# Performance work log

Measured on AMD Instinct MI355X. Metric: run time of the kernel, lower is better.

Reference implementation:

```python
import jax, jax.numpy as jnp
from jax import lax
import numpy as np

DIM = 128
HEADS = 2
WS = 4            # window_size = int(44 / 11)
HIDDEN = 4 * DIM  # ffn_expansion_factor = 4


def setup_inputs() -> dict:
    key = jax.random.key(0)
    ks = jax.random.split(key, 16)
    b, c, h, w = 4, DIM, 88, 88
    s = 0.02
    return {
        "x": jax.random.normal(ks[0], (b, c, h, w), jnp.float32),
        "mask": jax.random.uniform(ks[1], (b, 1, 44, 44), jnp.float32),
        "edge_f": jax.random.normal(ks[2], (b, c, 44, 44), jnp.float32),
        "ln1_w": jnp.ones((c,), jnp.float32),
        "ln1_b": jnp.zeros((c,), jnp.float32),
        "Wq": jax.random.normal(ks[3], (c, c), jnp.float32) * s,
        "Wk": jax.random.normal(ks[4], (c, c), jnp.float32) * s,
        "Wv": jax.random.normal(ks[5], (c, c), jnp.float32) * s,
        "ln2_w": jnp.ones((c,), jnp.float32),
        "ln2_b": jnp.zeros((c,), jnp.float32),
        "w_in": jax.random.normal(ks[6], (2 * HIDDEN, c), jnp.float32) * s,      # 1x1 conv dim -> 2*hidden
        "w_dw": jax.random.normal(ks[7], (2 * HIDDEN, 1, 3, 3), jnp.float32) * s,  # depthwise 3x3
        "w_out": jax.random.normal(ks[8], (c, HIDDEN), jnp.float32) * s,          # 1x1 conv hidden -> dim
    }


def _layernorm_c(t, g, beta):
    # WithBias LayerNorm over the channel axis (to_3d normalizes last dim == c)
    mu = t.mean(axis=1, keepdims=True)
    var = t.var(axis=1, keepdims=True)
    return (t - mu) / jnp.sqrt(var + 1e-5) * g[None, :, None, None] + beta[None, :, None, None]


def _windows(t, ws):
    # (b,c,h,w) -> (b*h*w/ws^2, ws^2, c), matching torch view/permute/contiguous
    b, c, h, w = t.shape
    t = t.reshape(b, c, h // ws, ws, w // ws, ws)
    t = t.transpose(0, 2, 4, 3, 5, 1)  # b, h/ws, w/ws, ws, ws, c
    return t.reshape(-1, ws * ws, c)


def reference(x, mask, edge_f, ln1_w, ln1_b, Wq, Wk, Wv, ln2_w, ln2_b, w_in, w_dw, w_out):
    b, c, h, w = x.shape
    ws, heads = WS, HEADS
    dh = c // heads
    scale = dh ** (-0.5)

    # ---- Attention branch (norm1 -> windowed edge/mask-conditioned attention) ----
    xn = _layernorm_c(x, ln1_w, ln1_b)
    edge = jax.image.resize(edge_f, (b, c, h, w), method="bilinear")
    m = jax.image.resize(mask, (b, mask.shape[1], h, w), method="bilinear")

    q = _windows(edge, ws) @ Wq.T            # (Bw, ws^2, c); dropout inactive (eval)
    x0 = _windows(xn * m, ws)                # mask-modulated keys/values
    k = x0 @ Wk.T
    v = x0 @ Wv.T

    Bw = q.shape[0]
    q = q.reshape(Bw, ws * ws, heads, dh)
    k = k.reshape(Bw, ws * ws, heads, dh)
    v = v.reshape(Bw, ws * ws, heads, dh)

    # dots: per-token head_dim x head_dim matrix, summed over heads (as in the source einsum)
    dots = jnp.einsum("bnhj,bnhk->bnjk", q, k) * scale   # (Bw, ws^2, dh, dh)
    attn = jax.nn.softmax(dots, axis=-1)
    out = jnp.einsum("bnjk,bnhk->bnhj", attn, v)          # (Bw, ws^2, heads, dh)

    out = out.reshape(Bw, ws * ws, c)
    out = out.reshape(b, h // ws, w // ws, ws * ws * c)
    out = out.transpose(0, 3, 1, 2).reshape(b, c, h, w)   # scrambled view, faithful to source

    x = x + out

    # ---- FeedForward branch (norm2 -> gated dwconv FFN) ----
    xn2 = _layernorm_c(x, ln2_w, ln2_b)
    t = jnp.einsum("oc,bchw->bohw", w_in, xn2)            # 1x1 conv, no bias
    t = lax.conv_general_dilated(
        t, w_dw, (1, 1), "SAME",
        feature_group_count=w_dw.shape[0],
        dimension_numbers=("NCHW", "OIHW", "NCHW"))
    t1, t2 = jnp.split(t, 2, axis=1)
    t = jax.nn.gelu(t1, approximate=False) * t2
    out2 = jnp.einsum("oc,bchw->bohw", w_out, t)
    return x + out2
```

## Files before the change

### kernel.cpp

```cpp
#include <hip/hip_runtime.h>
#include <hip/hip_bf16.h>
#include <math.h>

#define BATCH 4
#define C 128
#define H 88
#define W 88
#define HW 7744
#define NPIX 30976
#define HALF 44
#define HID 512

#if defined(__has_builtin)
#  if __has_builtin(__builtin_amdgcn_exp2f)
#    define EXP_FAST(x) __builtin_amdgcn_exp2f(x)
#    define QSCALE 0.18033688011112042f
#  endif
#endif
#ifndef EXP_FAST
#  define EXP_FAST(x) __expf(x)
#  define QSCALE 0.125f
#endif

typedef __attribute__((ext_vector_type(8))) short bfrag;
typedef __attribute__((ext_vector_type(4))) float f32x4;

__device__ __forceinline__ short f2bf(float f) {
    union { __hip_bfloat16 b; unsigned short u; } cv;
    cv.b = __float2bfloat16(f);
    return (short)cv.u;
}
__device__ __forceinline__ float bf2f(short s) {
    union { unsigned int u; float f; } cv;
    cv.u = ((unsigned int)(unsigned short)s) << 16;
    return cv.f;
}
__device__ __forceinline__ bfrag cvt8(const float* p) {
    const float4 f0 = *(const float4*)p;
    const float4 f1 = *(const float4*)(p + 4);
    bfrag t;
    t[0] = f2bf(f0.x); t[1] = f2bf(f0.y); t[2] = f2bf(f0.z); t[3] = f2bf(f0.w);
    t[4] = f2bf(f1.x); t[5] = f2bf(f1.y); t[6] = f2bf(f1.z); t[7] = f2bf(f1.w);
    return t;
}

__device__ __forceinline__ void up_taps(int i, int& j0, int& j1, float& w0, float& w1) {
    float f = 0.5f * i - 0.25f;
    int i0 = (int)floorf(f);
    float fr = f - (float)i0;
    j0 = max(i0, 0);
    j1 = min(i0 + 1, HALF - 1);
    w0 = 1.f - fr;
    w1 = fr;
}

__global__ __launch_bounds__(256) void k_pre(
    const float* __restrict__ x, const float* __restrict__ mask,
    const float* __restrict__ edge, const float* __restrict__ ln1w,
    const float* __restrict__ ln1b,
    __hip_bfloat16* __restrict__ xnm, __hip_bfloat16* __restrict__ eo)
{
    __shared__ float redS[8][32], redQ[8][32];
    const int tid = threadIdx.x, s = tid >> 5, px = tid & 31;
    const int blk = blockIdx.x, b = blk / 242, hw0 = (blk % 242) * 32;
    const int hw = hw0 + px, hi = hw / W, wi = hw % W;
    const int cs = s * 16;

    int y0, y1, x0, x1c; float wy0, wy1, wx0, wx1;
    up_taps(hi, y0, y1, wy0, wy1);
    up_taps(wi, x0, x1c, wx0, wx1);

    const float* mb = mask + (size_t)b * HALF * HALF;
    const float mval = wy0 * (wx0 * mb[y0 * HALF + x0] + wx1 * mb[y0 * HALF + x1c])
                     + wy1 * (wx0 * mb[y1 * HALF + x0] + wx1 * mb[y1 * HALF + x1c]);

    const float* xb = x + (size_t)b * C * HW;
    const float* ebs = edge + (size_t)b * C * HALF * HALF;
    float xr[16], er[16];
    float sum = 0.f, sq = 0.f;
    #pragma unroll
    for (int i = 0; i < 16; ++i) {
        const int c = cs + i;
        const float t = xb[c * HW + hw];
        xr[i] = t; sum += t; sq += t * t;
        const float* ec = ebs + c * HALF * HALF;
        er[i] = wy0 * (wx0 * ec[y0 * HALF + x0] + wx1 * ec[y0 * HALF + x1c])
              + wy1 * (wx0 * ec[y1 * HALF + x0] + wx1 * ec[y1 * HALF + x1c]);
    }
    redS[s][px] = sum; redQ[s][px] = sq;
    __syncthreads();
    float tsum = 0.f, tsq = 0.f;
    #pragma unroll
    for (int i = 0; i < 8; ++i) { tsum += redS[i][px]; tsq += redQ[i][px]; }
    const float mu = tsum * (1.f / C);
    const float rstd = rsqrtf(tsq * (1.f / C) - mu * mu + 1e-5f);

    const size_t gp = (size_t)b * HW + hw;
    bfrag r0, r1;
    #pragma unroll
    for (int i = 0; i < 8; ++i) {
        r0[i] = f2bf(((xr[i] - mu) * rstd * ln1w[cs + i] + ln1b[cs + i]) * mval);
        r1[i] = f2bf(((xr[8 + i] - mu) * rstd * ln1w[cs + 8 + i] + ln1b[cs + 8 + i]) * mval);
    }
    *(bfrag*)((short*)xnm + gp * C + cs) = r0;
    *(bfrag*)((short*)xnm + gp * C + cs + 8) = r1;
    #pragma unroll
    for (int i = 0; i < 8; ++i) { r0[i] = f2bf(er[i]); r1[i] = f2bf(er[8 + i]); }
    *(bfrag*)((short*)eo + gp * C + cs) = r0;
    *(bfrag*)((short*)eo + gp * C + cs + 8) = r1;
}


__global__ __launch_bounds__(512) void k_gemmQKV(
    const __hip_bfloat16* __restrict__ eb, const __hip_bfloat16* __restrict__ xnm,
    const float* __restrict__ Wq, const float* __restrict__ Wk, const float* __restrict__ Wv,
    __hip_bfloat16* __restrict__ qb, __hip_bfloat16* __restrict__ kb,
    __hip_bfloat16* __restrict__ vb)
{
    __shared__ short Bs[64 * 136];
    const int mat = blockIdx.y >> 1;
    const int c0 = (blockIdx.y & 1) * 64;
    const __hip_bfloat16* A; const float* Wf; __hip_bfloat16* Out;
    if (mat == 0)      { A = eb;  Wf = Wq; Out = qb; }
    else if (mat == 1) { A = xnm; Wf = Wk; Out = kb; }
    else               { A = xnm; Wf = Wv; Out = vb; }

    const int tid = threadIdx.x;
    {
        const int sr = tid & 63, sq = tid >> 6;
        const float* wr = Wf + (size_t)(c0 + sr) * 128 + sq * 16;
        short* dstS = &Bs[sr * 136 + sq * 16];
        *(bfrag*)dstS = cvt8(wr);
        *(bfrag*)(dstS + 8) = cvt8(wr + 8);
    }
    __syncthreads();

    const int lane = tid & 63, wv = tid >> 6;
    const int wm = wv & 3, wn = wv >> 2;
    const int px0 = blockIdx.x * 128 + wm * 32;
    const int lcb = wn * 32;
    const int lr = lane & 15, lg = lane >> 4;
    const short* As = (const short*)A;

    f32x4 acc[2][2];
    #pragma unroll
    for (int i = 0; i < 2; ++i)
        #pragma unroll
        for (int j = 0; j < 2; ++j)
            #pragma unroll
            for (int r = 0; r < 4; ++r) acc[i][j][r] = 0.f;

    bfrag a_[4][2], b_[2][2];
    #pragma unroll
    for (int ks = 0; ks < 4; ++ks)
        #pragma unroll
        for (int mi = 0; mi < 2; ++mi)
            a_[ks][mi] = *(const bfrag*)(As + (size_t)(px0 + mi * 16 + lr) * 128 + ks * 32 + lg * 8);
    #pragma unroll
    for (int nj = 0; nj < 2; ++nj)
        b_[0][nj] = *(const bfrag*)&Bs[(lcb + nj * 16 + lr) * 136 + lg * 8];

    #pragma unroll
    for (int ks = 0; ks < 4; ++ks) {
        if (ks < 3) {
            #pragma unroll
            for (int nj = 0; nj < 2; ++nj)
                b_[(ks + 1) & 1][nj] = *(const bfrag*)&Bs[(lcb + nj * 16 + lr) * 136 + (ks + 1) * 32 + lg * 8];
        }
        #pragma unroll
        for (int mi = 0; mi < 2; ++mi)
            #pragma unroll
            for (int nj = 0; nj < 2; ++nj)
                acc[mi][nj] = __builtin_amdgcn_mfma_f32_16x16x32_bf16(a_[ks][mi], b_[ks & 1][nj], acc[mi][nj], 0, 0, 0);
    }
    short* Os = (short*)Out;
    #pragma unroll
    for (int mi = 0; mi < 2; ++mi)
        #pragma unroll
        for (int nj = 0; nj < 2; ++nj)
            #pragma unroll
            for (int r = 0; r < 4; ++r) {
                const int p = px0 + mi * 16 + lg * 4 + r;
                const int c = c0 + lcb + nj * 16 + lr;
                Os[(size_t)p * 128 + c] = f2bf(acc[mi][nj][r]);
            }
}

__global__ __launch_bounds__(512) void k_gemm128(
    const __hip_bfloat16* __restrict__ A,
    const float* __restrict__ Wf,
    __hip_bfloat16* __restrict__ Out,
    int passMode)
{
    __shared__ short Bs[64 * 136];
    const int lc0 = blockIdx.y * 64;
    const int gc0 = (lc0 < 256) ? passMode * 256 + lc0 : 512 + passMode * 256 + (lc0 - 256);
    const int tid = threadIdx.x;
    {
        const int sr = tid & 63, sq = tid >> 6;
        const float* wr = Wf + (size_t)(gc0 + sr) * 128 + sq * 16;
        short* dstS = &Bs[sr * 136 + sq * 16];
        *(bfrag*)dstS = cvt8(wr);
        *(bfrag*)(dstS + 8) = cvt8(wr + 8);
    }
    __syncthreads();

    const int lane = tid & 63, wv = tid >> 6;
    const int wm = wv & 3, wn = wv >> 2;
    const int px0 = blockIdx.x * 128 + wm * 32;
    const int lcb = wn * 32;
    const int lr = lane & 15, lg = lane >> 4;
    const short* As = (const short*)A;

    f32x4 acc[2][2];
    #pragma unroll
    for (int i = 0; i < 2; ++i)
        #pragma unroll
        for (int j = 0; j < 2; ++j)
            #pragma unroll
            for (int r = 0; r < 4; ++r) acc[i][j][r] = 0.f;

    bfrag a_[4][2], b_[2][2];
    #pragma unroll
    for (int ks = 0; ks < 4; ++ks)
        #pragma unroll
        for (int mi = 0; mi < 2; ++mi)
            a_[ks][mi] = *(const bfrag*)(As + (size_t)(px0 + mi * 16 + lr) * 128 + ks * 32 + lg * 8);
    #pragma unroll
    for (int nj = 0; nj < 2; ++nj)
        b_[0][nj] = *(const bfrag*)&Bs[(lcb + nj * 16 + lr) * 136 + lg * 8];

    #pragma unroll
    for (int ks = 0; ks < 4; ++ks) {
        if (ks < 3) {
            #pragma unroll
            for (int nj = 0; nj < 2; ++nj)
                b_[(ks + 1) & 1][nj] = *(const bfrag*)&Bs[(lcb + nj * 16 + lr) * 136 + (ks + 1) * 32 + lg * 8];
        }
        #pragma unroll
        for (int mi = 0; mi < 2; ++mi)
            #pragma unroll
            for (int nj = 0; nj < 2; ++nj)
                acc[mi][nj] = __builtin_amdgcn_mfma_f32_16x16x32_bf16(a_[ks][mi], b_[ks & 1][nj], acc[mi][nj], 0, 0, 0);
    }
    short* Os = (short*)Out;
    #pragma unroll
    for (int mi = 0; mi < 2; ++mi)
        #pragma unroll
        for (int nj = 0; nj < 2; ++nj)
            #pragma unroll
            for (int r = 0; r < 4; ++r) {
                const int p = px0 + mi * 16 + lg * 4 + r;
                const int c = lc0 + lcb + nj * 16 + lr;
                Os[(size_t)p * 512 + c] = f2bf(acc[mi][nj][r]);
            }
}

__global__ __launch_bounds__(512) void k_attn2(
    const __hip_bfloat16* __restrict__ Q, const __hip_bfloat16* __restrict__ Kb,
    const __hip_bfloat16* __restrict__ Vb, const float* __restrict__ x,
    const float* __restrict__ ln2w, const float* __restrict__ ln2b,
    __hip_bfloat16* __restrict__ x1, __hip_bfloat16* __restrict__ xn2)
{
    __shared__ float kv[64][32][4];
    __shared__ float redS[16][32], redQ[16][32];
    const int tid = threadIdx.x, s = tid >> 5, px = tid & 31;
    const int blk = blockIdx.x, b = blk / 242, hw0 = (blk % 242) * 32;
    const int hw = hw0 + px, hi = hw / W, wi = hw % W;
    const size_t gp = (size_t)b * HW + hw;
    const int cs = s * 8;

    {
        const short* ks_ = (const short*)Kb + gp * C + cs;
        const short* vs_ = (const short*)Vb + gp * C + cs;
        bfrag kb0 = *(const bfrag*)ks_;
        bfrag vb0 = *(const bfrag*)vs_;
        const int comp = (s < 8) ? 0 : 1;
        const int kkb = (s & 7) * 8;
        #pragma unroll
        for (int i = 0; i < 8; ++i) {
            kv[kkb + i][px][comp]     = bf2f(kb0[i]);
            kv[kkb + i][px][comp + 2] = bf2f(vb0[i]);
        }
    }
    float q1r[4], q2r[4];
    {
        const short* qs = (const short*)Q + gp * C;
        #pragma unroll
        for (int rr = 0; rr < 4; ++rr) {
            const int j = s + 16 * rr;
            q1r[rr] = bf2f(qs[j]) * QSCALE;
            q2r[rr] = bf2f(qs[64 + j]) * QSCALE;
        }
    }
    __syncthreads();

    float ssum[4], o1[4], o2[4];
    #pragma unroll
    for (int rr = 0; rr < 4; ++rr) { ssum[rr] = 0.f; o1[rr] = 0.f; o2[rr] = 0.f; }

    #pragma unroll 8
    for (int kk = 0; kk < 64; ++kk) {
        const f32x4 vv = *(const f32x4*)kv[kk][px];
        #pragma unroll
        for (int rr = 0; rr < 4; ++rr) {
            const float d = q1r[rr] * vv[0] + q2r[rr] * vv[1];
            const float e = EXP_FAST(d);
            ssum[rr] += e;
            o1[rr] += e * vv[2];
            o2[rr] += e * vv[3];
        }
    }

    const int r_ = hi >> 2, col = wi >> 2, n = (hi & 3) * 4 + (wi & 3);
    const size_t bbase = (size_t)b * C * HW;
    const int wbase = r_ * 22 + col;
    float v1r[4], v2r[4];
    float sum = 0.f, sq = 0.f;
    #pragma unroll
    for (int rr = 0; rr < 4; ++rr) {
        const int j = s + 16 * rr;
        const float inv = 1.f / ssum[rr];
        const int f1 = (n * C + j) * 484 + wbase;
        const int f2 = (n * C + 64 + j) * 484 + wbase;
        const float v1 = x[bbase + f1] + o1[rr] * inv;
        const float v2 = x[bbase + f2] + o2[rr] * inv;
        x1[bbase + f1] = __float2bfloat16(v1);
        x1[bbase + f2] = __float2bfloat16(v2);
        v1r[rr] = v1; v2r[rr] = v2;
        sum += v1 + v2; sq += v1 * v1 + v2 * v2;
    }
    __syncthreads();
    float (*vT)[32] = reinterpret_cast<float(*)[32]>(&kv[0][0][0]);
    #pragma unroll
    for (int rr = 0; rr < 4; ++rr) {
        const int j = s + 16 * rr;
        vT[j][px] = v1r[rr];
        vT[64 + j][px] = v2r[rr];
    }
    redS[s][px] = sum; redQ[s][px] = sq;
    __syncthreads();
    float tsum = 0.f, tsq = 0.f;
    #pragma unroll
    for (int i = 0; i < 16; ++i) { tsum += redS[i][px]; tsq += redQ[i][px]; }
    const float mu = tsum * (1.f / C);
    const float rstd = rsqrtf(tsq * (1.f / C) - mu * mu + 1e-5f);
    bfrag r0;
    #pragma unroll
    for (int i = 0; i < 8; ++i)
        r0[i] = f2bf((vT[cs + i][px] - mu) * rstd * ln2w[cs + i] + ln2b[cs + i]);
    *(bfrag*)((short*)xn2 + gp * C + cs) = r0;
}

__global__ __launch_bounds__(256) void k_dw(
    const __hip_bfloat16* __restrict__ U,
    const float* __restrict__ wdw,
    __hip_bfloat16* __restrict__ Gout,
    int pass)
{
    const int cl = threadIdx.x;
    const int blk = blockIdx.x;
    const int seg = blk % 11;
    const int hi = (blk / 11) % H;
    const int b = blk / (11 * H);
    const int w0 = seg * 8;
    const int gc1 = pass * 256 + cl, gc2 = 512 + gc1;

    float w1[9], w2[9];
    #pragma unroll
    for (int t = 0; t < 9; ++t) { w1[t] = wdw[gc1 * 9 + t]; w2[t] = wdw[gc2 * 9 + t]; }

    const short* Us = (const short*)U;
    const size_t base = (size_t)b * HW;
    const bool r0ok = (hi - 1) >= 0, r2ok = (hi + 1) < H;

    float A1[3][3], A2[3][3];

    #define LOADCOL(slot, wc)  do {                                              \
        if ((unsigned)(wc) >= W) {                                               \
            A1[slot][0]=A1[slot][1]=A1[slot][2]=0.f;                             \
            A2[slot][0]=A2[slot][1]=A2[slot][2]=0.f;                             \
        } else {                                                                 \
            size_t p1 = base + (size_t)(hi - 1) * W + (wc);                      \
            size_t p2 = base + (size_t)hi * W + (wc);                            \
            size_t p3 = base + (size_t)(hi + 1) * W + (wc);                      \
            A1[slot][0] = r0ok ? bf2f(Us[p1 * 512 + cl]) : 0.f;                  \
            A2[slot][0] = r0ok ? bf2f(Us[p1 * 512 + 256 + cl]) : 0.f;            \
            A1[slot][1] = bf2f(Us[p2 * 512 + cl]);                               \
            A2[slot][1] = bf2f(Us[p2 * 512 + 256 + cl]);                         \
            A1[slot][2] = r2ok ? bf2f(Us[p3 * 512 + cl]) : 0.f;                  \
            A2[slot][2] = r2ok ? bf2f(Us[p3 * 512 + 256 + cl]) : 0.f;            \
        } } while (0)

    LOADCOL(0, w0 - 1);
    LOADCOL(1, w0);

    #pragma unroll
    for (int i = 0; i < 8; ++i) {
        const int wi = w0 + i;
        const int sl = i % 3, sm = (i + 1) % 3, sr = (i + 2) % 3;
        LOADCOL(sr, wi + 1);
        float t1 = 0.f, t2 = 0.f;
        #pragma unroll
        for (int r = 0; r < 3; ++r) {
            t1 += w1[r * 3 + 0] * A1[sl][r] + w1[r * 3 + 1] * A1[sm][r] + w1[r * 3 + 2] * A1[sr][r];
            t2 += w2[r * 3 + 0] * A2[sl][r] + w2[r * 3 + 1] * A2[sm][r] + w2[r * 3 + 2] * A2[sr][r];
        }
        const float gl = 0.5f * t1 * (1.f + erff(t1 * 0.70710678118654752f));
        Gout[(base + (size_t)hi * W + wi) * 512 + pass * 256 + cl] = __float2bfloat16(gl * t2);
    }
    #undef LOADCOL
}

__global__ __launch_bounds__(512) void k_gemm512(
    const __hip_bfloat16* __restrict__ G,
    const float* __restrict__ Wof,
    const __hip_bfloat16* __restrict__ X1,
    float* __restrict__ Outp)
{
    __shared__ short Bs[64 * 520];
    const int c0 = blockIdx.y * 64;
    const int tid = threadIdx.x;
    {
        const int sr = tid & 63, sq = tid >> 6;
        const float* wr = Wof + (size_t)(c0 + sr) * 512 + sq * 64;
        short* dstS = &Bs[sr * 520 + sq * 64];
        #pragma unroll
        for (int i8 = 0; i8 < 8; ++i8)
            *(bfrag*)(dstS + i8 * 8) = cvt8(wr + i8 * 8);
    }
    __syncthreads();

    const int lane = tid & 63, wv = tid >> 6;
    const int wm = wv & 3, wn = wv >> 2;
    const int px0 = blockIdx.x * 128 + wm * 32;
    const int lcb = wn * 32;
    const int lr = lane & 15, lg = lane >> 4;
    const short* Gs = (const short*)G;

    f32x4 acc[2][2];
    #pragma unroll
    for (int i = 0; i < 2; ++i)
        #pragma unroll
        for (int j = 0; j < 2; ++j)
            #pragma unroll
            for (int r = 0; r < 4; ++r) acc[i][j][r] = 0.f;

    bfrag a_[4][2], b_[2][2];
    #pragma unroll
    for (int ks = 0; ks < 4; ++ks)
        #pragma unroll
        for (int mi = 0; mi < 2; ++mi)
            a_[ks][mi] = *(const bfrag*)(Gs + (size_t)(px0 + mi * 16 + lr) * 512 + ks * 32 + lg * 8);
    #pragma unroll
    for (int nj = 0; nj < 2; ++nj)
        b_[0][nj] = *(const bfrag*)&Bs[(lcb + nj * 16 + lr) * 520 + lg * 8];

    #pragma unroll
    for (int ks = 0; ks < 16; ++ks) {
        if (ks < 15) {
            #pragma unroll
            for (int nj = 0; nj < 2; ++nj)
                b_[(ks + 1) & 1][nj] = *(const bfrag*)&Bs[(lcb + nj * 16 + lr) * 520 + (ks + 1) * 32 + lg * 8];
        }
        if (ks < 12) {
            #pragma unroll
            for (int mi = 0; mi < 2; ++mi)
                a_[(ks + 4) & 3][mi] = *(const bfrag*)(Gs + (size_t)(px0 + mi * 16 + lr) * 512 + (ks + 4) * 32 + lg * 8);
        }
        #pragma unroll
        for (int mi = 0; mi < 2; ++mi)
            #pragma unroll
            for (int nj = 0; nj < 2; ++nj)
                acc[mi][nj] = __builtin_amdgcn_mfma_f32_16x16x32_bf16(a_[ks & 3][mi], b_[ks & 1][nj], acc[mi][nj], 0, 0, 0);
    }

    #pragma unroll
    for (int mi = 0; mi < 2; ++mi)
        #pragma unroll
        for (int nj = 0; nj < 2; ++nj)
            #pragma unroll
            for (int r = 0; r < 4; ++r) {
                const int p = px0 + mi * 16 + lg * 4 + r;
                const int c = c0 + lcb + nj * 16 + lr;
                const int b = p / HW, hw = p % HW;
                const size_t idx = ((size_t)b * C + c) * HW + hw;
                Outp[idx] = __bfloat162float(X1[idx]) + acc[mi][nj][r];
            }
}

extern "C" void kernel_launch(void* const* d_in, const int* in_sizes, int n_in,
                              void* d_out, int out_size, void* d_ws, size_t ws_size,
                              hipStream_t stream) {
    (void)in_sizes; (void)n_in; (void)out_size; (void)ws_size;
    const float* x     = (const float*)d_in[0];
    const float* mask  = (const float*)d_in[1];
    const float* edge  = (const float*)d_in[2];
    const float* ln1w  = (const float*)d_in[3];
    const float* ln1b  = (const float*)d_in[4];
    const float* Wq    = (const float*)d_in[5];
    const float* Wk    = (const float*)d_in[6];
    const float* Wv    = (const float*)d_in[7];
    const float* ln2w  = (const float*)d_in[8];
    const float* ln2b  = (const float*)d_in[9];
    const float* w_in  = (const float*)d_in[10];
    const float* w_dw  = (const float*)d_in[11];
    const float* w_out = (const float*)d_in[12];
    float* out = (float*)d_out;

    char* ws = (char*)d_ws;
    __hip_bfloat16* x1  = (__hip_bfloat16*)(ws + 0);
    __hip_bfloat16* xn2 = (__hip_bfloat16*)(ws + 7929856);
    __hip_bfloat16* uh  = (__hip_bfloat16*)(ws + 15859712);
    __hip_bfloat16* g   = (__hip_bfloat16*)(ws + 47579136);
    __hip_bfloat16* qb  = (__hip_bfloat16*)(ws + 15859712);
    __hip_bfloat16* kb  = (__hip_bfloat16*)(ws + 23789568);
    __hip_bfloat16* vb  = (__hip_bfloat16*)(ws + 31719424);
    __hip_bfloat16* eb  = (__hip_bfloat16*)(ws + 39649280);
    __hip_bfloat16* xnm = (__hip_bfloat16*)(ws + 47579136);

    k_pre<<<968, 256, 0, stream>>>(x, mask, edge, ln1w, ln1b, xnm, eb);
    k_gemmQKV<<<dim3(242, 6), 512, 0, stream>>>(eb, xnm, Wq, Wk, Wv, qb, kb, vb);
    k_attn2<<<968, 512, 0, stream>>>(qb, kb, vb, x, ln2w, ln2b, x1, xn2);
    k_gemm128<<<dim3(242, 8), 512, 0, stream>>>(xn2, w_in, uh, 0);
    k_dw<<<3872, 256, 0, stream>>>(uh, w_dw, g, 0);
    k_gemm128<<<dim3(242, 8), 512, 0, stream>>>(xn2, w_in, uh, 1);
    k_dw<<<3872, 256, 0, stream>>>(uh, w_dw, g, 1);
    k_gemm512<<<dim3(242, 2), 512, 0, stream>>>(g, w_out, x1, out);
}
```

Measured before the change: 222.1 us.

## Store FFN intermediate as fp8-e5m2, merge passes, split attention residual

The 1x1 conv output (1024 channels) is now stored as 8-bit e5m2 values produced by truncating fp16 with round-to-nearest-even. This halves its footprint and lets the two-pass gemm128/dwconv sequence become a single pass over all channels. The attention kernel now writes its output pixel-contiguously to a scratch buffer, and a separate residual+LayerNorm kernel gathers it with the scrambled permutation. The residual kernel's x reads and x1 writes are coalesced across pixels, which the old scattered channel-major accesses were not. This adds a kernel launch and an extra round-trip for the attention output, and e5m2 storage loses substantial precision on the intermediate activations.

```diff
diff --git a/kernel.cpp b/kernel.cpp
--- a/kernel.cpp
+++ b/kernel.cpp
@@ -1,5 +1,6 @@
 #include <hip/hip_runtime.h>
 #include <hip/hip_bf16.h>
+#include <hip/hip_fp16.h>
 #include <math.h>
 
 #define BATCH 4
@@ -44,6 +45,20 @@
     return t;
 }
 
+__device__ __forceinline__ unsigned char f2e5(float f) {
+    union { __half h; unsigned short u; } cv;
+    cv.h = __float2half(f);
+    unsigned short lo = cv.u & 0xFF;
+    unsigned short hi = cv.u >> 8;
+    hi += (lo > 0x80 || (lo == 0x80 && (hi & 1))) ? 1 : 0;
+    return (unsigned char)hi;
+}
+__device__ __forceinline__ float e52f(unsigned char b) {
+    union { unsigned short u; __half h; } cv;
+    cv.u = ((unsigned short)b) << 8;
+    return __half2float(cv.h);
+}
+
 __device__ __forceinline__ void up_taps(int i, int& j0, int& j1, float& w0, float& w1) {
     float f = 0.5f * i - 0.25f;
     int i0 = (int)floorf(f);
@@ -189,12 +204,10 @@
 __global__ __launch_bounds__(512) void k_gemm128(
     const __hip_bfloat16* __restrict__ A,
     const float* __restrict__ Wf,
-    __hip_bfloat16* __restrict__ Out,
-    int passMode)
+    unsigned char* __restrict__ Out)
 {
     __shared__ short Bs[64 * 136];
-    const int lc0 = blockIdx.y * 64;
-    const int gc0 = (lc0 < 256) ? passMode * 256 + lc0 : 512 + passMode * 256 + (lc0 - 256);
+    const int gc0 = blockIdx.y * 64;
     const int tid = threadIdx.x;
     {
         const int sr = tid & 63, sq = tid >> 6;
@@ -243,7 +256,6 @@
             for (int nj = 0; nj < 2; ++nj)
                 acc[mi][nj] = __builtin_amdgcn_mfma_f32_16x16x32_bf16(a_[ks][mi], b_[ks & 1][nj], acc[mi][nj], 0, 0, 0);
     }
-    short* Os = (short*)Out;
     #pragma unroll
     for (int mi = 0; mi < 2; ++mi)
         #pragma unroll
@@ -251,23 +263,19 @@
             #pragma unroll
             for (int r = 0; r < 4; ++r) {
                 const int p = px0 + mi * 16 + lg * 4 + r;
-                const int c = lc0 + lcb + nj * 16 + lr;
-                Os[(size_t)p * 512 + c] = f2bf(acc[mi][nj][r]);
+                const int c = gc0 + lcb + nj * 16 + lr;
+                Out[(size_t)p * 1024 + c] = f2e5(acc[mi][nj][r]);
             }
 }
 
-__global__ __launch_bounds__(512) void k_attn2(
+__global__ __launch_bounds__(512) void k_attn3(
     const __hip_bfloat16* __restrict__ Q, const __hip_bfloat16* __restrict__ Kb,
-    const __hip_bfloat16* __restrict__ Vb, const float* __restrict__ x,
-    const float* __restrict__ ln2w, const float* __restrict__ ln2b,
-    __hip_bfloat16* __restrict__ x1, __hip_bfloat16* __restrict__ xn2)
+    const __hip_bfloat16* __restrict__ Vb, __hip_bfloat16* __restrict__ att)
 {
     __shared__ float kv[64][32][4];
-    __shared__ float redS[16][32], redQ[16][32];
     const int tid = threadIdx.x, s = tid >> 5, px = tid & 31;
     const int blk = blockIdx.x, b = blk / 242, hw0 = (blk % 242) * 32;
-    const int hw = hw0 + px, hi = hw / W, wi = hw % W;
-    const size_t gp = (size_t)b * HW + hw;
+    const size_t gp = (size_t)b * HW + hw0 + px;
     const int cs = s * 8;
 
     {
@@ -311,52 +319,76 @@
             o2[rr] += e * vv[3];
         }
     }
-
-    const int r_ = hi >> 2, col = wi >> 2, n = (hi & 3) * 4 + (wi & 3);
-    const size_t bbase = (size_t)b * C * HW;
-    const int wbase = r_ * 22 + col;
-    float v1r[4], v2r[4];
-    float sum = 0.f, sq = 0.f;
+    __syncthreads();
+    float* vTT = &kv[0][0][0];
     #pragma unroll
     for (int rr = 0; rr < 4; ++rr) {
         const int j = s + 16 * rr;
         const float inv = 1.f / ssum[rr];
-        const int f1 = (n * C + j) * 484 + wbase;
-        const int f2 = (n * C + 64 + j) * 484 + wbase;
-        const float v1 = x[bbase + f1] + o1[rr] * inv;
-        const float v2 = x[bbase + f2] + o2[rr] * inv;
-        x1[bbase + f1] = __float2bfloat16(v1);
-        x1[bbase + f2] = __float2bfloat16(v2);
-        v1r[rr] = v1; v2r[rr] = v2;
-        sum += v1 + v2; sq += v1 * v1 + v2 * v2;
-    }
-    __syncthreads();
-    float (*vT)[32] = reinterpret_cast<float(*)[32]>(&kv[0][0][0]);
-    #pragma unroll
-    for (int rr = 0; rr < 4; ++rr) {
-        const int j = s + 16 * rr;
-        vT[j][px] = v1r[rr];
-        vT[64 + j][px] = v2r[rr];
+        vTT[px * 137 + j]      = o1[rr] * inv;
+        vTT[px * 137 + 64 + j] = o2[rr] * inv;
+    }
+    __syncthreads();
+    const int pxw = tid >> 4, c8 = (tid & 15) * 8;
+    const size_t gpw = (size_t)b * HW + hw0 + pxw;
+    bfrag r0;
+    #pragma unroll
+    for (int i = 0; i < 8; ++i) r0[i] = f2bf(vTT[pxw * 137 + c8 + i]);
+    *(bfrag*)((short*)att + gpw * C + c8) = r0;
+}
+
+__global__ __launch_bounds__(256) void k_resid(
+    const float* __restrict__ x, const __hip_bfloat16* __restrict__ att,
+    const float* __restrict__ ln2w, const float* __restrict__ ln2b,
+    __hip_bfloat16* __restrict__ x1, __hip_bfloat16* __restrict__ xn2)
+{
+    __shared__ float redS[8][32], redQ[8][32];
+    const int tid = threadIdx.x, s = tid >> 5, px = tid & 31;
+    const int blk = blockIdx.x, b = blk / 242, hw0 = (blk % 242) * 32;
+    const int hw = hw0 + px;
+    const int cs = s * 16;
+    const int q = hw / 484, wbase = hw - q * 484;
+    const int r_ = wbase / 22, col = wbase - r_ * 22;
+    const short* attS = (const short*)att;
+    const size_t bb = (size_t)b * HW;
+
+    float v[16];
+    float sum = 0.f, sq = 0.f;
+    #pragma unroll
+    for (int i = 0; i < 16; ++i) {
+        const int c = cs + i;
+        const int n = c >> 3;
+        const int cj = 16 * (c & 7) + q;
+        const int shi = r_ * 4 + (n >> 2), swi = col * 4 + (n & 3);
+        const size_t gps = bb + (size_t)shi * W + swi;
+        const float o = bf2f(attS[gps * C + cj]);
+        const float xv = x[((size_t)b * C + c) * HW + hw];
+        const float vv = xv + o;
+        v[i] = vv; sum += vv; sq += vv * vv;
+        x1[((size_t)b * C + c) * HW + hw] = __float2bfloat16(vv);
     }
     redS[s][px] = sum; redQ[s][px] = sq;
     __syncthreads();
     float tsum = 0.f, tsq = 0.f;
     #pragma unroll
-    for (int i = 0; i < 16; ++i) { tsum += redS[i][px]; tsq += redQ[i][px]; }
+    for (int i = 0; i < 8; ++i) { tsum += redS[i][px]; tsq += redQ[i][px]; }
     const float mu = tsum * (1.f / C);
     const float rstd = rsqrtf(tsq * (1.f / C) - mu * mu + 1e-5f);
-    bfrag r0;
-    #pragma unroll
-    for (int i = 0; i < 8; ++i)
-        r0[i] = f2bf((vT[cs + i][px] - mu) * rstd * ln2w[cs + i] + ln2b[cs + i]);
+    const size_t gp = bb + hw;
+    bfrag r0, r1;
+    #pragma unroll
+    for (int i = 0; i < 8; ++i) {
+        r0[i] = f2bf((v[i] - mu) * rstd * ln2w[cs + i] + ln2b[cs + i]);
+        r1[i] = f2bf((v[8 + i] - mu) * rstd * ln2w[cs + 8 + i] + ln2b[cs + 8 + i]);
+    }
     *(bfrag*)((short*)xn2 + gp * C + cs) = r0;
-}
-
-__global__ __launch_bounds__(256) void k_dw(
-    const __hip_bfloat16* __restrict__ U,
+    *(bfrag*)((short*)xn2 + gp * C + cs + 8) = r1;
+}
+
+__global__ __launch_bounds__(512) void k_dw(
+    const unsigned char* __restrict__ U,
     const float* __restrict__ wdw,
-    __hip_bfloat16* __restrict__ Gout,
-    int pass)
+    __hip_bfloat16* __restrict__ Gout)
 {
     const int cl = threadIdx.x;
     const int blk = blockIdx.x;
@@ -364,13 +396,12 @@
     const int hi = (blk / 11) % H;
     const int b = blk / (11 * H);
     const int w0 = seg * 8;
-    const int gc1 = pass * 256 + cl, gc2 = 512 + gc1;
+    const int gc1 = cl, gc2 = 512 + cl;
 
     float w1[9], w2[9];
     #pragma unroll
     for (int t = 0; t < 9; ++t) { w1[t] = wdw[gc1 * 9 + t]; w2[t] = wdw[gc2 * 9 + t]; }
 
-    const short* Us = (const short*)U;
     const size_t base = (size_t)b * HW;
     const bool r0ok = (hi - 1) >= 0, r2ok = (hi + 1) < H;
 
@@ -384,12 +415,12 @@
             size_t p1 = base + (size_t)(hi - 1) * W + (wc);                      \
             size_t p2 = base + (size_t)hi * W + (wc);                            \
             size_t p3 = base + (size_t)(hi + 1) * W + (wc);                      \
-            A1[slot][0] = r0ok ? bf2f(Us[p1 * 512 + cl]) : 0.f;                  \
-            A2[slot][0] = r0ok ? bf2f(Us[p1 * 512 + 256 + cl]) : 0.f;            \
-            A1[slot][1] = bf2f(Us[p2 * 512 + cl]);                               \
-            A2[slot][1] = bf2f(Us[p2 * 512 + 256 + cl]);                         \
-            A1[slot][2] = r2ok ? bf2f(Us[p3 * 512 + cl]) : 0.f;                  \
-            A2[slot][2] = r2ok ? bf2f(Us[p3 * 512 + 256 + cl]) : 0.f;            \
+            A1[slot][0] = r0ok ? e52f(U[p1 * 1024 + cl]) : 0.f;                  \
+            A2[slot][0] = r0ok ? e52f(U[p1 * 1024 + 512 + cl]) : 0.f;            \
+            A1[slot][1] = e52f(U[p2 * 1024 + cl]);                               \
+            A2[slot][1] = e52f(U[p2 * 1024 + 512 + cl]);                         \
+            A1[slot][2] = r2ok ? e52f(U[p3 * 1024 + cl]) : 0.f;                  \
+            A2[slot][2] = r2ok ? e52f(U[p3 * 1024 + 512 + cl]) : 0.f;            \
         } } while (0)
 
     LOADCOL(0, w0 - 1);
@@ -407,7 +438,7 @@
             t2 += w2[r * 3 + 0] * A2[sl][r] + w2[r * 3 + 1] * A2[sm][r] + w2[r * 3 + 2] * A2[sr][r];
         }
         const float gl = 0.5f * t1 * (1.f + erff(t1 * 0.70710678118654752f));
-        Gout[(base + (size_t)hi * W + wi) * 512 + pass * 256 + cl] = __float2bfloat16(gl * t2);
+        Gout[(base + (size_t)hi * W + wi) * 512 + cl] = __float2bfloat16(gl * t2);
     }
     #undef LOADCOL
 }
@@ -511,20 +542,20 @@
     char* ws = (char*)d_ws;
     __hip_bfloat16* x1  = (__hip_bfloat16*)(ws + 0);
     __hip_bfloat16* xn2 = (__hip_bfloat16*)(ws + 7929856);
-    __hip_bfloat16* uh  = (__hip_bfloat16*)(ws + 15859712);
+    unsigned char*  u8  = (unsigned char*)(ws + 15859712);
     __hip_bfloat16* g   = (__hip_bfloat16*)(ws + 47579136);
     __hip_bfloat16* qb  = (__hip_bfloat16*)(ws + 15859712);
     __hip_bfloat16* kb  = (__hip_bfloat16*)(ws + 23789568);
     __hip_bfloat16* vb  = (__hip_bfloat16*)(ws + 31719424);
     __hip_bfloat16* eb  = (__hip_bfloat16*)(ws + 39649280);
+    __hip_bfloat16* att = (__hip_bfloat16*)(ws + 39649280);
     __hip_bfloat16* xnm = (__hip_bfloat16*)(ws + 47579136);
 
     k_pre<<<968, 256, 0, stream>>>(x, mask, edge, ln1w, ln1b, xnm, eb);
     k_gemmQKV<<<dim3(242, 6), 512, 0, stream>>>(eb, xnm, Wq, Wk, Wv, qb, kb, vb);
-    k_attn2<<<968, 512, 0, stream>>>(qb, kb, vb, x, ln2w, ln2b, x1, xn2);
-    k_gemm128<<<dim3(242, 8), 512, 0, stream>>>(xn2, w_in, uh, 0);
-    k_dw<<<3872, 256, 0, stream>>>(uh, w_dw, g, 0);
-    k_gemm128<<<dim3(242, 8), 512, 0, stream>>>(xn2, w_in, uh, 1);
-    k_dw<<<3872, 256, 0, stream>>>(uh, w_dw, g, 1);
+    k_attn3<<<968, 512, 0, stream>>>(qb, kb, vb, att);
+    k_resid<<<968, 256, 0, stream>>>(x, att, ln2w, ln2b, x1, xn2);
+    k_gemm128<<<dim3(242, 16), 512, 0, stream>>>(xn2, w_in, u8);
+    k_dw<<<3872, 512, 0, stream>>>(u8, w_dw, g);
     k_gemm512<<<dim3(242, 2), 512, 0, stream>>>(g, w_out, x1, out);
 }
```

After: 228.7 us. +3.0%, slower.
